# Kernel optimization log

Measured on AMD Instinct MI355X. Metric: run time of the kernel, lower is better.

The kernel has to match this reference:

```python
import jax, jax.numpy as jnp
import numpy as np

L, H, E, FFN, V, BLOCK = 8, 16, 1024, 4096, 32000, 2048
D = E // H  # head dim = 64
EPS = 1e-5
STD = 0.02

def _ln(x, g, b):
    m = jnp.mean(x, axis=-1, keepdims=True)
    v = jnp.var(x, axis=-1, keepdims=True)
    return (x - m) * jax.lax.rsqrt(v + EPS) * g + b

def setup_inputs() -> dict:
    key = jax.random.key(0)
    ks = jax.random.split(key, 12)
    n = lambda k, shape: (jax.random.normal(k, shape, dtype=jnp.float32) * STD)
    return {
        "idx": jax.random.randint(ks[0], (2, 2048), 0, V),
        "tok_emb": n(ks[1], (V, E)),
        "pos_emb": n(ks[2], (BLOCK, E)),
        # attention weights stored [in, out] so we use x @ W
        "wq": n(ks[3], (L, E, E)),
        "wk": n(ks[4], (L, E, E)),
        "wv": n(ks[5], (L, E, E)),
        "wo": n(ks[6], (L, E, E)),
        "bo": jnp.zeros((L, E), jnp.float32),
        "w1": n(ks[7], (L, E, FFN)),
        "b1": jnp.zeros((L, FFN), jnp.float32),
        "w2": n(ks[8], (L, FFN, E)),
        "b2": jnp.zeros((L, E), jnp.float32),
        "ln1_g": jnp.ones((L, E), jnp.float32),
        "ln1_b": jnp.zeros((L, E), jnp.float32),
        "ln2_g": jnp.ones((L, E), jnp.float32),
        "ln2_b": jnp.zeros((L, E), jnp.float32),
        "lnf_g": jnp.ones((E,), jnp.float32),
        "lnf_b": jnp.zeros((E,), jnp.float32),
    }

def reference(idx, tok_emb, pos_emb, wq, wk, wv, wo, bo, w1, b1, w2, b2,
              ln1_g, ln1_b, ln2_g, ln2_b, lnf_g, lnf_b):
    B, T = idx.shape
    x = tok_emb[idx] + pos_emb[:T]  # [B,T,E]
    causal = jnp.tril(jnp.ones((T, T), dtype=bool))
    scale = 1.0 / np.sqrt(D)

    def step(x, p):
        (wq_, wk_, wv_, wo_, bo_, w1_, b1_, w2_, b2_,
         g1, be1, g2, be2) = p
        h = _ln(x, g1, be1)
        q = (h @ wq_).reshape(B, T, H, D)
        k = (h @ wk_).reshape(B, T, H, D)
        v = (h @ wv_).reshape(B, T, H, D)
        scores = jnp.einsum('bthd,bshd->bhts', q, k) * scale  # [B,H,T,T]
        scores = jnp.where(causal, scores, -jnp.inf)
        w = jax.nn.softmax(scores, axis=-1)
        attn = jnp.einsum('bhts,bshd->bthd', w, v).reshape(B, T, E)
        x = x + attn @ wo_ + bo_
        h2 = _ln(x, g2, be2)
        x = x + jax.nn.relu(h2 @ w1_ + b1_) @ w2_ + b2_
        return x, None

    x, _ = jax.lax.scan(step, x, (wq, wk, wv, wo, bo, w1, b1, w2, b2,
                                  ln1_g, ln1_b, ln2_g, ln2_b))
    x = _ln(x, lnf_g, lnf_b)
    logits = x @ tok_emb.T  # tied weights
    return logits
```

## Files before the change

### kernel.cpp

```cpp
#include <hip/hip_runtime.h>
#include <hip/hip_bf16.h>
#include <cstdint>
#include <cstddef>

#define LAYERS   8
#define HEADS    16
#define EMB      1024
#define FFND     4096
#define VOCAB    32000
#define SEQ      2048
#define NBATCH   2
#define MROWS    (NBATCH*SEQ)
#define HDIM     64
#define QKVSTR   3072
#define LN_EPS   1e-5f
#define QSCALE   0.18033688011112042f

typedef __hip_bfloat16 bf16;
typedef short short8 __attribute__((ext_vector_type(8)));
typedef float f32x4  __attribute__((ext_vector_type(4)));

__device__ __forceinline__ void async_copy16(const bf16* g, bf16* l) {
  __builtin_amdgcn_global_load_lds(
      (const __attribute__((address_space(1))) void*)g,
      (__attribute__((address_space(3))) void*)l, 16, 0, 0);
}

__device__ __forceinline__ uint32_t bfbits(float x) {
  __hip_bfloat16 h = __float2bfloat16(x);
  return (uint32_t)reinterpret_cast<uint16_t&>(h);
}

struct __align__(8) B4 { bf16 a, b, c, d; };

__global__ void k_f32_to_bf16(const float* __restrict__ in, bf16* __restrict__ out, long n4) {
  long i = (long)blockIdx.x * blockDim.x + threadIdx.x;
  const long stride = (long)gridDim.x * blockDim.x;
  for (; i < n4; i += stride) {
    float4 v = reinterpret_cast<const float4*>(in)[i];
    B4 o;
    o.a = __float2bfloat16(v.x);
    o.b = __float2bfloat16(v.y);
    o.c = __float2bfloat16(v.z);
    o.d = __float2bfloat16(v.w);
    reinterpret_cast<B4*>(out)[i] = o;
  }
}

__global__ void k_embed(const int* __restrict__ idx, const float* __restrict__ tok,
                        const float* __restrict__ pos, float* __restrict__ x) {
  const int row  = blockIdx.x;
  const int tpos = row & (SEQ - 1);
  const int token = idx[row];
  const float4* te = (const float4*)(tok + (long)token * EMB);
  const float4* pe = (const float4*)(pos + (long)tpos * EMB);
  float4* xo = (float4*)(x + (long)row * EMB);
  for (int i = threadIdx.x; i < EMB / 4; i += blockDim.x) {
    float4 a = te[i], b = pe[i];
    a.x += b.x; a.y += b.y; a.z += b.z; a.w += b.w;
    xo[i] = a;
  }
}

__global__ void k_transpose_all(const float* __restrict__ wq, const float* __restrict__ wk,
                                const float* __restrict__ wv, const float* __restrict__ wo,
                                const float* __restrict__ w1, const float* __restrict__ w2,
                                bf16* __restrict__ qkvT, bf16* __restrict__ woT,
                                bf16* __restrict__ w1T, bf16* __restrict__ w2T) {
  __shared__ float tile[32][33];
  const int bid = blockIdx.x;
  const float* in; bf16* out; int K, N, bx, by;
  if (bid < 4096) {
    const int rest = bid & 1023;
    switch (bid >> 10) {
      case 0:  in = wq; out = qkvT;                 break;
      case 1:  in = wk; out = qkvT + EMB * EMB;     break;
      case 2:  in = wv; out = qkvT + 2 * EMB * EMB; break;
      default: in = wo; out = woT;                  break;
    }
    K = EMB; N = EMB; bx = rest & 31; by = rest >> 5;
  } else if (bid < 8192) {
    const int rest = bid - 4096;
    in = w1; out = w1T; K = EMB; N = FFND;
    bx = rest & 127; by = rest >> 7;
  } else {
    const int rest = bid - 8192;
    in = w2; out = w2T; K = FFND; N = EMB;
    bx = rest & 31; by = rest >> 5;
  }
  const int n0 = bx * 32, k0 = by * 32;
  const int tx = threadIdx.x, ty = threadIdx.y;
  for (int i = 0; i < 32; i += 8)
    tile[ty + i][tx] = in[(long)(k0 + ty + i) * N + n0 + tx];
  __syncthreads();
  for (int i = 0; i < 32; i += 8)
    out[(long)(n0 + ty + i) * K + k0 + tx] = __float2bfloat16(tile[tx][ty + i]);
}

__global__ void k_transpose_v(const bf16* __restrict__ v, int vstr, bf16* __restrict__ vt) {
  __shared__ bf16 tile[32][33];
  const int bh = blockIdx.z;
  const int b = bh >> 4, h = bh & 15;
  const int t0 = blockIdx.x * 32, d0 = blockIdx.y * 32;
  const int tx = threadIdx.x, ty = threadIdx.y;
  for (int i = 0; i < 32; i += 8)
    tile[ty + i][tx] = v[(long)(b * SEQ + t0 + ty + i) * vstr + h * HDIM + d0 + tx];
  __syncthreads();
  for (int i = 0; i < 32; i += 8)
    vt[(long)(bh * HDIM + d0 + ty + i) * SEQ + t0 + tx] = tile[tx][ty + i];
}

__global__ __launch_bounds__(256)
void k_layernorm(const float* __restrict__ x, const float* __restrict__ g,
                 const float* __restrict__ b, bf16* __restrict__ out) {
  const int wid  = threadIdx.x >> 6;
  const int lane = threadIdx.x & 63;
  const long row = (long)blockIdx.x * 4 + wid;
  const float4* xr = (const float4*)(x + row * EMB);
  float4 xv[4];
  float s = 0.f, sq = 0.f;
#pragma unroll
  for (int i = 0; i < 4; i++) {
    xv[i] = xr[lane + i * 64];
    s  += xv[i].x + xv[i].y + xv[i].z + xv[i].w;
    sq += xv[i].x * xv[i].x + xv[i].y * xv[i].y + xv[i].z * xv[i].z + xv[i].w * xv[i].w;
  }
#pragma unroll
  for (int m = 1; m < 64; m <<= 1) { s += __shfl_xor(s, m); sq += __shfl_xor(sq, m); }
  const float mean = s * (1.f / EMB);
  const float var  = sq * (1.f / EMB) - mean * mean;
  const float rstd = rsqrtf(var + LN_EPS);
  const float4* gv = (const float4*)g;
  const float4* bv = (const float4*)b;
  bf16* orow = out + row * EMB;
#pragma unroll
  for (int i = 0; i < 4; i++) {
    const int c4 = lane + i * 64;
    const float4 gg = gv[c4], bb = bv[c4];
    uint2 o;
    o.x = (bfbits((xv[i].y - mean) * rstd * gg.y + bb.y) << 16) |
           bfbits((xv[i].x - mean) * rstd * gg.x + bb.x);
    o.y = (bfbits((xv[i].w - mean) * rstd * gg.w + bb.w) << 16) |
           bfbits((xv[i].z - mean) * rstd * gg.z + bb.z);
    *reinterpret_cast<uint2*>(&orow[c4 * 4]) = o;
  }
}

template<int MODE>
__global__ __launch_bounds__(512, 2)
void gemm256(const bf16* __restrict__ A, const bf16* __restrict__ Bt,
             int M, int N, int K,
             bf16* __restrict__ outB, float* __restrict__ outF,
             const float* __restrict__ bias) {
  extern __shared__ __align__(16) char smem[];
  char* const smA = smem;
  char* const smB = smem + 65536;

  const int t    = threadIdx.x;
  const int lane = t & 63;
  const int wid  = t >> 6;
  const int wr   = wid >> 2;
  const int wc   = wid & 3;
  const int lrow = lane & 15;
  const int ks16 = (lane >> 4) * 16;
  const int rswz = (lrow & 7) << 4;

  int lin = blockIdx.x * gridDim.y + blockIdx.y;
  { const int nwg = gridDim.x * gridDim.y; const int per = nwg >> 3;
    lin = (lin & 7) * per + (lin >> 3); }
  const int gx8  = gridDim.x * 8;
  const int half = lin / gx8;
  const int rem  = lin - half * gx8;
  const long bm  = (long)(half * 8 + (rem & 7)) * 256;
  const long bn  = (long)(rem >> 3) * 256;
  const int NT = K >> 6;

  const int row0 = wid * 8 + (lane >> 3);
  const int col0 = ((lane & 7) ^ (lane >> 3)) * 8;
  const int row1 = row0 + 64;
  const int dst0 = wid * 1024;
  const int dst1 = 8192 + wid * 1024;
  const bf16* const gA = A  + bm * K;
  const bf16* const gB = Bt + bn * K;

  auto STG = [&](char* ring, const bf16* g_, int tile, int h) {
    char* slot = ring + (((tile << 1) + h) & 3) * 16384;
    const bf16* sb = g_ + ((long)h * 128) * K + (long)tile * 64;
    async_copy16(sb + (long)row0 * K + col0, (bf16*)(slot + dst0));
    async_copy16(sb + (long)row1 * K + col0, (bf16*)(slot + dst1));
  };
  auto LDA8 = [&](int u, int m, int kk) -> short8 {
    const int off = (m * 16 + lrow) * 128 + ((kk * 64 + ks16) ^ rswz);
    return *reinterpret_cast<const short8*>(smA + (((u << 1) + wr) & 3) * 16384 + off);
  };
  auto LDB8 = [&](int u, int n, int kk) -> short8 {
    const int off = ((wc & 1) * 64 + n * 16 + lrow) * 128 + ((kk * 64 + ks16) ^ rswz);
    return *reinterpret_cast<const short8*>(smB + (((u << 1) + (wc >> 1)) & 3) * 16384 + off);
  };
#define MF(a_, b_, c_) __builtin_amdgcn_mfma_f32_16x16x32_bf16(a_, b_, c_, 0, 0, 0)

  f32x4 acc[8][4] = {};

  STG(smB, gB, 0, 0); STG(smB, gB, 0, 1);
  STG(smA, gA, 0, 0); STG(smA, gA, 0, 1);
  STG(smB, gB, 1, 0); STG(smB, gB, 1, 1);
  asm volatile("s_waitcnt vmcnt(4)" ::: "memory");
  __builtin_amdgcn_s_barrier();

  short8 bq[4][2];
  for (int u = 0; u < NT; u++) {
#pragma unroll
    for (int n = 0; n < 4; n++) { bq[n][0] = LDB8(u, n, 0); bq[n][1] = LDB8(u, n, 1); }
    short8 a0 = LDA8(u, 0, 0), a1 = LDA8(u, 0, 1), a2 = LDA8(u, 1, 0), a3 = LDA8(u, 1, 1);
    if (u + 1 < NT) STG(smA, gA, u + 1, 0);
    __builtin_amdgcn_s_barrier();
    asm volatile("s_waitcnt lgkmcnt(0)" ::: "memory");
    __builtin_amdgcn_sched_barrier(0);
    __builtin_amdgcn_s_setprio(1);
#pragma unroll
    for (int n = 0; n < 4; n++) {
      acc[0][n] = MF(a0, bq[n][0], acc[0][n]); acc[0][n] = MF(a1, bq[n][1], acc[0][n]);
      acc[1][n] = MF(a2, bq[n][0], acc[1][n]); acc[1][n] = MF(a3, bq[n][1], acc[1][n]);
    }
    __builtin_amdgcn_s_setprio(0);
    __builtin_amdgcn_s_barrier();

    a0 = LDA8(u, 2, 0); a1 = LDA8(u, 2, 1); a2 = LDA8(u, 3, 0); a3 = LDA8(u, 3, 1);
    if (u + 1 < NT) STG(smA, gA, u + 1, 1);
    __builtin_amdgcn_s_barrier();
    asm volatile("s_waitcnt lgkmcnt(0)" ::: "memory");
    __builtin_amdgcn_sched_barrier(0);
    __builtin_amdgcn_s_setprio(1);
#pragma unroll
    for (int n = 0; n < 4; n++) {
      acc[2][n] = MF(a0, bq[n][0], acc[2][n]); acc[2][n] = MF(a1, bq[n][1], acc[2][n]);
      acc[3][n] = MF(a2, bq[n][0], acc[3][n]); acc[3][n] = MF(a3, bq[n][1], acc[3][n]);
    }
    __builtin_amdgcn_s_setprio(0);
    __builtin_amdgcn_s_barrier();

    a0 = LDA8(u, 4, 0); a1 = LDA8(u, 4, 1); a2 = LDA8(u, 5, 0); a3 = LDA8(u, 5, 1);
    if (u + 2 < NT) STG(smB, gB, u + 2, 0);
    __builtin_amdgcn_s_barrier();
    asm volatile("s_waitcnt lgkmcnt(0)" ::: "memory");
    __builtin_amdgcn_sched_barrier(0);
    __builtin_amdgcn_s_setprio(1);
#pragma unroll
    for (int n = 0; n < 4; n++) {
      acc[4][n] = MF(a0, bq[n][0], acc[4][n]); acc[4][n] = MF(a1, bq[n][1], acc[4][n]);
      acc[5][n] = MF(a2, bq[n][0], acc[5][n]); acc[5][n] = MF(a3, bq[n][1], acc[5][n]);
    }
    __builtin_amdgcn_s_setprio(0);
    __builtin_amdgcn_s_barrier();

    a0 = LDA8(u, 6, 0); a1 = LDA8(u, 6, 1); a2 = LDA8(u, 7, 0); a3 = LDA8(u, 7, 1);
    if (u + 2 < NT) STG(smB, gB, u + 2, 1);
    __builtin_amdgcn_s_barrier();
    asm volatile("s_waitcnt lgkmcnt(0)" ::: "memory");
    __builtin_amdgcn_sched_barrier(0);
    __builtin_amdgcn_s_setprio(1);
#pragma unroll
    for (int n = 0; n < 4; n++) {
      acc[6][n] = MF(a0, bq[n][0], acc[6][n]); acc[6][n] = MF(a1, bq[n][1], acc[6][n]);
      acc[7][n] = MF(a2, bq[n][0], acc[7][n]); acc[7][n] = MF(a3, bq[n][1], acc[7][n]);
    }
    __builtin_amdgcn_s_setprio(0);
    if (u + 2 < NT) { asm volatile("s_waitcnt vmcnt(4)" ::: "memory"); }
    else            { asm volatile("s_waitcnt vmcnt(0)" ::: "memory"); }
    __builtin_amdgcn_s_barrier();
  }

  const long rb = bm + wr * 128 + (lane >> 4) * 4;
  const long cb = bn + wc * 64 + lrow;
#pragma unroll
  for (int m = 0; m < 8; m++) {
#pragma unroll
    for (int n = 0; n < 4; n++) {
      const long col = cb + n * 16;
#pragma unroll
      for (int r = 0; r < 4; r++) {
        const long row = rb + m * 16 + r;
        float v = acc[m][n][r];
        if (MODE == 0) {
          if (col < EMB) v *= QSCALE;
          outB[row * N + col] = __float2bfloat16(v);
        } else if (MODE == 2) {
          v += bias[col];
          outB[row * N + col] = __float2bfloat16(v > 0.f ? v : 0.f);
        } else {
          outF[row * N + col] = v;
        }
      }
    }
  }
#undef MF
}

#define BM 128
#define BN 128
#define BK 32

__global__ __launch_bounds__(256)
void gemm_bt(const bf16* __restrict__ A, const bf16* __restrict__ Bt,
             int M, int N, int K,
             float* __restrict__ outF, const float* __restrict__ bias) {
  __shared__ __align__(16) bf16 lA[2][BM * BK];
  __shared__ __align__(16) bf16 lB[2][BN * BK];
  const int t    = threadIdx.x;
  const int lane = t & 63;
  const int wid  = t >> 6;
  const int wr   = wid >> 1;
  const int wc   = wid & 1;
  const long bm  = (long)blockIdx.y * BM;
  const long bn  = (long)blockIdx.x * BN;
  const int  kz  = blockIdx.z;
  const int  Kh  = K >> 1;

  f32x4 acc[4][4] = {};

  const long arow = t >> 2;
  const int  acol = (((t & 3) ^ ((t >> 2) & 3)) * 8);
  const bf16* gA = A  + (bm + arow) * K + kz * Kh + acol;
  const bf16* gB = Bt + (bn + arow) * K + kz * Kh + acol;
  const long astep = 64L * K;

  auto STGBT = [&](int buf, int k0) {
    async_copy16(gA + k0,         &lA[buf][wid * 512]);
    async_copy16(gA + k0 + astep, &lA[buf][wid * 512 + 2048]);
    async_copy16(gB + k0,         &lB[buf][wid * 512]);
    async_copy16(gB + k0 + astep, &lB[buf][wid * 512 + 2048]);
  };

  STGBT(0, 0);
  __syncthreads();

  int cur = 0;
  for (int k0 = 0; k0 < Kh; k0 += BK) {
    if (k0 + BK < Kh) STGBT(cur ^ 1, k0 + BK);

    const int ksel = (((lane >> 4) ^ (lane & 3)) * 8);
    short8 af[4], bfv[4];
#pragma unroll
    for (int i = 0; i < 4; i++) {
      af[i]  = *reinterpret_cast<const short8*>(&lA[cur][(wr * 64 + i * 16 + (lane & 15)) * BK + ksel]);
      bfv[i] = *reinterpret_cast<const short8*>(&lB[cur][(wc * 64 + i * 16 + (lane & 15)) * BK + ksel]);
    }
#pragma unroll
    for (int i = 0; i < 4; i++)
#pragma unroll
      for (int j = 0; j < 4; j++)
        acc[i][j] = __builtin_amdgcn_mfma_f32_16x16x32_bf16(af[i], bfv[j], acc[i][j], 0, 0, 0);
    __syncthreads();
    cur ^= 1;
  }

  const long rbase = bm + wr * 64 + (lane >> 4) * 4;
  const long cbase = bn + wc * 64 + (lane & 15);
#pragma unroll
  for (int i = 0; i < 4; i++) {
#pragma unroll
    for (int j = 0; j < 4; j++) {
      const long col = cbase + j * 16;
      const float bv = kz ? 0.f : bias[col];
#pragma unroll
      for (int r = 0; r < 4; r++) {
        const long row = rbase + i * 16 + r;
        unsafeAtomicAdd(&outF[row * N + col], acc[i][j][r] + bv);
      }
    }
  }
}

__global__ __launch_bounds__(256)
void k_attn(const bf16* __restrict__ qkv, const bf16* __restrict__ vt, bf16* __restrict__ o) {
  const int bh = blockIdx.y;
  const int qt = (bh & 16) ? blockIdx.x : (gridDim.x - 1 - blockIdx.x);
  const int b  = bh >> 4;
  const int h  = bh & 15;
  const int t0b = qt * 128;
  const int tid = threadIdx.x;
  const int w    = tid >> 6;
  const int lane = tid & 63;
  const int lg = lane >> 4;
  const int li = lane & 15;
  const int t0w = t0b + w * 32;

  __shared__ __align__(16) bf16 Kl[2][64 * 64];
  __shared__ __align__(16) bf16 Vl[2][64 * 64];
  __shared__ __align__(16) bf16 Pl[4][32 * 64];

  const bf16* qbase = qkv + (long)(b * SEQ) * QKVSTR + h * HDIM;
  const bf16* kbase = qkv + (long)(b * SEQ) * QKVSTR + EMB + h * HDIM;
  const bf16* vbase = vt + (long)bh * HDIM * SEQ;

  short8 qf[2][2];
#pragma unroll
  for (int f = 0; f < 2; f++) {
    const bf16* qrow = qbase + (long)(t0w + f * 16 + li) * QKVSTR;
    qf[f][0] = *reinterpret_cast<const short8*>(&qrow[lg * 8]);
    qf[f][1] = *reinterpret_cast<const short8*>(&qrow[32 + lg * 8]);
  }

  f32x4 oacc[2][4] = {};
  float mrow[2] = {-1e30f, -1e30f}, lrow[2] = {0.f, 0.f};

  const int nkt = (t0b >> 6) + 1;
  const int l8  = lane >> 3;
  const int sl8 = ((lane & 7) ^ l8) * 8;

  char* const Pw = (char*)&Pl[w][0];
  const int pswz = (li & 7) << 4;

#pragma unroll
  for (int sh = 0; sh < 2; sh++) {
    const int r = sh * 32 + w * 8 + l8;
    async_copy16(kbase + (long)r * QKVSTR + sl8, &Kl[0][(sh * 32 + w * 8) * 64]);
    async_copy16(vbase + (long)r * SEQ + sl8,    &Vl[0][(sh * 32 + w * 8) * 64]);
  }
  __syncthreads();

  int cur = 0;
  for (int kt = 0; kt <= nkt; kt++) {
    const int s0 = kt * 64;
    if (kt < nkt) {
      const int s0n = s0 + 64;
      bf16* Kn = &Kl[cur ^ 1][0];
      bf16* Vn = &Vl[cur ^ 1][0];
#pragma unroll
      for (int sh = 0; sh < 2; sh++) {
        const int r = sh * 32 + w * 8 + l8;
        async_copy16(kbase + (long)(s0n + r) * QKVSTR + sl8, Kn + (sh * 32 + w * 8) * 64);
        async_copy16(vbase + (long)r * SEQ + s0n + sl8,      Vn + (sh * 32 + w * 8) * 64);
      }
    }

    f32x4 s[2][4] = {};
#pragma unroll
    for (int kk = 0; kk < 2; kk++)
#pragma unroll
      for (int sf = 0; sf < 4; sf++) {
        const short8 kf = *reinterpret_cast<const short8*>(
            &Kl[cur][(sf * 16 + li) * 64 + ((((kk << 2) | lg) ^ (li & 7)) * 8)]);
        s[0][sf] = __builtin_amdgcn_mfma_f32_16x16x32_bf16(kf, qf[0][kk], s[0][sf], 0, 0, 0);
        s[1][sf] = __builtin_amdgcn_mfma_f32_16x16x32_bf16(kf, qf[1][kk], s[1][sf], 0, 0, 0);
      }

    const bool diag = (kt >= nkt - 1);
    if (diag) {
#pragma unroll
      for (int f = 0; f < 2; f++)
#pragma unroll
        for (int sf = 0; sf < 4; sf++)
#pragma unroll
          for (int r = 0; r < 4; r++)
            if (s0 + sf * 16 + lg * 4 + r > t0w + f * 16 + li) s[f][sf][r] = -1e30f;
    }

#pragma unroll
    for (int f = 0; f < 2; f++) {
      float mx = -1e30f;
#pragma unroll
      for (int sf = 0; sf < 4; sf++)
        mx = fmaxf(mx, fmaxf(fmaxf(s[f][sf][0], s[f][sf][1]), fmaxf(s[f][sf][2], s[f][sf][3])));
      mx = fmaxf(mx, __shfl_xor(mx, 16));
      mx = fmaxf(mx, __shfl_xor(mx, 32));
      if (__any(mx > mrow[f] + 8.f)) {
        const float mnew = fmaxf(mrow[f], mx);
        const float alpha = exp2f(mrow[f] - mnew);
        mrow[f] = mnew;
        lrow[f] *= alpha;
#pragma unroll
        for (int d = 0; d < 4; d++)
#pragma unroll
          for (int r = 0; r < 4; r++) oacc[f][d][r] *= alpha;
      }
      float rs = 0.f;
#pragma unroll
      for (int sf = 0; sf < 4; sf++)
#pragma unroll
        for (int r = 0; r < 4; r++) {
          const float pv = exp2f(s[f][sf][r] - mrow[f]);
          s[f][sf][r] = pv;
          rs += pv;
        }
      rs += __shfl_xor(rs, 16);
      rs += __shfl_xor(rs, 32);
      lrow[f] += rs;

#pragma unroll
      for (int sf = 0; sf < 4; sf++) {
        uint2 pw2;
        pw2.x = (bfbits(s[f][sf][1]) << 16) | bfbits(s[f][sf][0]);
        pw2.y = (bfbits(s[f][sf][3]) << 16) | bfbits(s[f][sf][2]);
        *reinterpret_cast<uint2*>(Pw + (f * 16 + li) * 128 + ((sf * 32 + lg * 8) ^ pswz)) = pw2;
      }
    }

#pragma unroll
    for (int kk = 0; kk < 2; kk++) {
      const short8 pb0 = *reinterpret_cast<const short8*>(
          Pw + li * 128 + ((kk * 64 + lg * 16) ^ pswz));
      const short8 pb1 = *reinterpret_cast<const short8*>(
          Pw + (16 + li) * 128 + ((kk * 64 + lg * 16) ^ pswz));
#pragma unroll
      for (int d = 0; d < 4; d++) {
        const short8 vf = *reinterpret_cast<const short8*>(
            &Vl[cur][(d * 16 + li) * 64 + ((((kk << 2) | lg) ^ (li & 7)) * 8)]);
        oacc[0][d] = __builtin_amdgcn_mfma_f32_16x16x32_bf16(vf, pb0, oacc[0][d], 0, 0, 0);
        oacc[1][d] = __builtin_amdgcn_mfma_f32_16x16x32_bf16(vf, pb1, oacc[1][d], 0, 0, 0);
      }
    }

    __syncthreads();
    cur ^= 1;
  }

#pragma unroll
  for (int f = 0; f < 2; f++) {
    const float inv = 1.f / lrow[f];
    bf16* orow = o + (long)(b * SEQ + t0w + f * 16 + li) * EMB + h * HDIM;
#pragma unroll
    for (int d = 0; d < 4; d++) {
      uint2 ow;
      ow.x = (bfbits(oacc[f][d][1] * inv) << 16) | bfbits(oacc[f][d][0] * inv);
      ow.y = (bfbits(oacc[f][d][3] * inv) << 16) | bfbits(oacc[f][d][2] * inv);
      *reinterpret_cast<uint2*>(&orow[d * 16 + lg * 4]) = ow;
    }
  }
}

extern "C" void kernel_launch(void* const* d_in, const int* in_sizes, int n_in,
                              void* d_out, int out_size, void* d_ws, size_t ws_size,
                              hipStream_t stream) {
  (void)in_sizes; (void)n_in; (void)out_size; (void)ws_size;
  const int*   idx = (const int*)  d_in[0];
  const float* tok = (const float*)d_in[1];
  const float* pos = (const float*)d_in[2];
  const float* wq  = (const float*)d_in[3];
  const float* wk  = (const float*)d_in[4];
  const float* wv  = (const float*)d_in[5];
  const float* wo  = (const float*)d_in[6];
  const float* bo  = (const float*)d_in[7];
  const float* w1  = (const float*)d_in[8];
  const float* b1  = (const float*)d_in[9];
  const float* w2  = (const float*)d_in[10];
  const float* b2  = (const float*)d_in[11];
  const float* g1  = (const float*)d_in[12];
  const float* be1 = (const float*)d_in[13];
  const float* g2  = (const float*)d_in[14];
  const float* be2 = (const float*)d_in[15];
  const float* gf  = (const float*)d_in[16];
  const float* bef = (const float*)d_in[17];
  float* out = (float*)d_out;

  (void)hipFuncSetAttribute((const void*)gemm256<0>, hipFuncAttributeMaxDynamicSharedMemorySize, 131072);
  (void)hipFuncSetAttribute((const void*)gemm256<2>, hipFuncAttributeMaxDynamicSharedMemorySize, 131072);
  (void)hipFuncSetAttribute((const void*)gemm256<3>, hipFuncAttributeMaxDynamicSharedMemorySize, 131072);

  char* p = (char*)d_ws;
  auto take = [&p](size_t bytes) { char* r = p; p += (bytes + 255) & ~(size_t)255; return r; };
  float* xf   = (float*)take((size_t)MROWS * EMB * 4);
  bf16*  hb   = (bf16*) take((size_t)MROWS * EMB * 2);
  bf16*  qkvb = (bf16*) take((size_t)MROWS * QKVSTR * 2);
  bf16*  vtb  = (bf16*) take((size_t)MROWS * EMB * 2);
  bf16*  ab   = (bf16*) take((size_t)MROWS * EMB * 2);
  bf16*  fb   = (bf16*) take((size_t)MROWS * FFND * 2);
  bf16*  wqkvT= (bf16*) take((size_t)QKVSTR * EMB * 2);
  bf16*  woT  = (bf16*) take((size_t)EMB * EMB * 2);
  bf16*  w1T  = (bf16*) take((size_t)FFND * EMB * 2);
  bf16*  w2T  = (bf16*) take((size_t)EMB * FFND * 2);
  bf16*  tokT = (bf16*) take((size_t)VOCAB * EMB * 2);

  k_f32_to_bf16<<<2048, 256, 0, stream>>>(tok, tokT, (long)VOCAB * EMB / 4);
  k_embed<<<MROWS, 256, 0, stream>>>(idx, tok, pos, xf);

  const dim3 tb(32, 8);

  for (int l = 0; l < LAYERS; l++) {
    const size_t we = (size_t)l * EMB * EMB;
    const size_t wfo = (size_t)l * EMB * FFND;
    k_transpose_all<<<12288, tb, 0, stream>>>(
        wq + we, wk + we, wv + we, wo + we, w1 + wfo, w2 + wfo, wqkvT, woT, w1T, w2T);

    k_layernorm<<<MROWS / 4, 256, 0, stream>>>(xf, g1 + l * EMB, be1 + l * EMB, hb);
    gemm256<0><<<dim3(QKVSTR / 256, MROWS / 256), 512, 131072, stream>>>(
        hb, wqkvT, MROWS, QKVSTR, EMB, qkvb, nullptr, nullptr);
    k_transpose_v<<<dim3(SEQ / 32, HDIM / 32, NBATCH * HEADS), tb, 0, stream>>>(qkvb + 2 * EMB, QKVSTR, vtb);
    k_attn<<<dim3(SEQ / 128, NBATCH * HEADS), 256, 0, stream>>>(qkvb, vtb, ab);
    gemm_bt<<<dim3(EMB / BN, MROWS / BM, 2), 256, 0, stream>>>(ab, woT, MROWS, EMB, EMB, xf, bo + l * EMB);
    k_layernorm<<<MROWS / 4, 256, 0, stream>>>(xf, g2 + l * EMB, be2 + l * EMB, hb);
    gemm256<2><<<dim3(FFND / 256, MROWS / 256), 512, 131072, stream>>>(
        hb, w1T, MROWS, FFND, EMB, fb, nullptr, b1 + l * FFND);
    gemm_bt<<<dim3(EMB / BN, MROWS / BM, 2), 256, 0, stream>>>(fb, w2T, MROWS, EMB, FFND, xf, b2 + l * EMB);
  }

  k_layernorm<<<MROWS / 4, 256, 0, stream>>>(xf, gf, bef, hb);
  gemm256<3><<<dim3(VOCAB / 256, MROWS / 256), 512, 131072, stream>>>(
      hb, tokT, MROWS, VOCAB, EMB, nullptr, out, nullptr);
}
```

Baseline: 2.557 ms.

## Halve GEMM barrier phases and process two N tiles per block in vocab GEMM

The 256x256 GEMM main loop now does two compute phases per K tile instead of four. Each phase loads eight A fragments, issues both A or both B half-tile prefetches together, and runs 32 MFMAs, which halves the number of barriers per iteration. A new NSUB template parameter lets one block loop over several consecutive 256-wide N tiles. The vocabulary projection uses it with two tiles per block, cutting the grid from 125 to 63 column groups. The price is more live A-fragment registers under a tight launch-bound budget, which risks spills, and a serial second tile in the logits GEMM that may change wave-quantization behaviour.

```diff
diff --git a/kernel.cpp b/kernel.cpp
--- a/kernel.cpp
+++ b/kernel.cpp
@@ -146,7 +146,7 @@
   }
 }
 
-template<int MODE>
+template<int MODE, int NSUB>
 __global__ __launch_bounds__(512, 2)
 void gemm256(const bf16* __restrict__ A, const bf16* __restrict__ Bt,
              int M, int N, int K,
@@ -172,7 +172,7 @@
   const int half = lin / gx8;
   const int rem  = lin - half * gx8;
   const long bm  = (long)(half * 8 + (rem & 7)) * 256;
-  const long bn  = (long)(rem >> 3) * 256;
+  const long bn0 = (long)(rem >> 3) * (256 * NSUB);
   const int NT = K >> 6;
 
   const int row0 = wid * 8 + (lane >> 3);
@@ -180,8 +180,7 @@
   const int row1 = row0 + 64;
   const int dst0 = wid * 1024;
   const int dst1 = 8192 + wid * 1024;
-  const bf16* const gA = A  + bm * K;
-  const bf16* const gB = Bt + bn * K;
+  const bf16* const gA = A + bm * K;
 
   auto STG = [&](char* ring, const bf16* g_, int tile, int h) {
     char* slot = ring + (((tile << 1) + h) & 3) * 16384;
@@ -199,96 +198,80 @@
   };
 #define MF(a_, b_, c_) __builtin_amdgcn_mfma_f32_16x16x32_bf16(a_, b_, c_, 0, 0, 0)
 
-  f32x4 acc[8][4] = {};
-
-  STG(smB, gB, 0, 0); STG(smB, gB, 0, 1);
-  STG(smA, gA, 0, 0); STG(smA, gA, 0, 1);
-  STG(smB, gB, 1, 0); STG(smB, gB, 1, 1);
-  asm volatile("s_waitcnt vmcnt(4)" ::: "memory");
-  __builtin_amdgcn_s_barrier();
-
-  short8 bq[4][2];
-  for (int u = 0; u < NT; u++) {
-#pragma unroll
-    for (int n = 0; n < 4; n++) { bq[n][0] = LDB8(u, n, 0); bq[n][1] = LDB8(u, n, 1); }
-    short8 a0 = LDA8(u, 0, 0), a1 = LDA8(u, 0, 1), a2 = LDA8(u, 1, 0), a3 = LDA8(u, 1, 1);
-    if (u + 1 < NT) STG(smA, gA, u + 1, 0);
+  for (int v = 0; v < NSUB; v++) {
+    const long bn = bn0 + (long)v * 256;
+    if (NSUB > 1 && bn >= N) break;
+    const bf16* const gB = Bt + bn * K;
+
+    f32x4 acc[8][4] = {};
+
+    STG(smB, gB, 0, 0); STG(smB, gB, 0, 1);
+    STG(smA, gA, 0, 0); STG(smA, gA, 0, 1);
+    STG(smB, gB, 1, 0); STG(smB, gB, 1, 1);
+    asm volatile("s_waitcnt vmcnt(4)" ::: "memory");
     __builtin_amdgcn_s_barrier();
-    asm volatile("s_waitcnt lgkmcnt(0)" ::: "memory");
-    __builtin_amdgcn_sched_barrier(0);
-    __builtin_amdgcn_s_setprio(1);
-#pragma unroll
-    for (int n = 0; n < 4; n++) {
-      acc[0][n] = MF(a0, bq[n][0], acc[0][n]); acc[0][n] = MF(a1, bq[n][1], acc[0][n]);
-      acc[1][n] = MF(a2, bq[n][0], acc[1][n]); acc[1][n] = MF(a3, bq[n][1], acc[1][n]);
-    }
-    __builtin_amdgcn_s_setprio(0);
-    __builtin_amdgcn_s_barrier();
-
-    a0 = LDA8(u, 2, 0); a1 = LDA8(u, 2, 1); a2 = LDA8(u, 3, 0); a3 = LDA8(u, 3, 1);
-    if (u + 1 < NT) STG(smA, gA, u + 1, 1);
-    __builtin_amdgcn_s_barrier();
-    asm volatile("s_waitcnt lgkmcnt(0)" ::: "memory");
-    __builtin_amdgcn_sched_barrier(0);
-    __builtin_amdgcn_s_setprio(1);
-#pragma unroll
-    for (int n = 0; n < 4; n++) {
-      acc[2][n] = MF(a0, bq[n][0], acc[2][n]); acc[2][n] = MF(a1, bq[n][1], acc[2][n]);
-      acc[3][n] = MF(a2, bq[n][0], acc[3][n]); acc[3][n] = MF(a3, bq[n][1], acc[3][n]);
-    }
-    __builtin_amdgcn_s_setprio(0);
-    __builtin_amdgcn_s_barrier();
-
-    a0 = LDA8(u, 4, 0); a1 = LDA8(u, 4, 1); a2 = LDA8(u, 5, 0); a3 = LDA8(u, 5, 1);
-    if (u + 2 < NT) STG(smB, gB, u + 2, 0);
-    __builtin_amdgcn_s_barrier();
-    asm volatile("s_waitcnt lgkmcnt(0)" ::: "memory");
-    __builtin_amdgcn_sched_barrier(0);
-    __builtin_amdgcn_s_setprio(1);
-#pragma unroll
-    for (int n = 0; n < 4; n++) {
-      acc[4][n] = MF(a0, bq[n][0], acc[4][n]); acc[4][n] = MF(a1, bq[n][1], acc[4][n]);
-      acc[5][n] = MF(a2, bq[n][0], acc[5][n]); acc[5][n] = MF(a3, bq[n][1], acc[5][n]);
-    }
-    __builtin_amdgcn_s_setprio(0);
-    __builtin_amdgcn_s_barrier();
-
-    a0 = LDA8(u, 6, 0); a1 = LDA8(u, 6, 1); a2 = LDA8(u, 7, 0); a3 = LDA8(u, 7, 1);
-    if (u + 2 < NT) STG(smB, gB, u + 2, 1);
-    __builtin_amdgcn_s_barrier();
-    asm volatile("s_waitcnt lgkmcnt(0)" ::: "memory");
-    __builtin_amdgcn_sched_barrier(0);
-    __builtin_amdgcn_s_setprio(1);
-#pragma unroll
-    for (int n = 0; n < 4; n++) {
-      acc[6][n] = MF(a0, bq[n][0], acc[6][n]); acc[6][n] = MF(a1, bq[n][1], acc[6][n]);
-      acc[7][n] = MF(a2, bq[n][0], acc[7][n]); acc[7][n] = MF(a3, bq[n][1], acc[7][n]);
-    }
-    __builtin_amdgcn_s_setprio(0);
-    if (u + 2 < NT) { asm volatile("s_waitcnt vmcnt(4)" ::: "memory"); }
-    else            { asm volatile("s_waitcnt vmcnt(0)" ::: "memory"); }
-    __builtin_amdgcn_s_barrier();
-  }
-
-  const long rb = bm + wr * 128 + (lane >> 4) * 4;
-  const long cb = bn + wc * 64 + lrow;
-#pragma unroll
-  for (int m = 0; m < 8; m++) {
-#pragma unroll
-    for (int n = 0; n < 4; n++) {
-      const long col = cb + n * 16;
-#pragma unroll
-      for (int r = 0; r < 4; r++) {
-        const long row = rb + m * 16 + r;
-        float v = acc[m][n][r];
-        if (MODE == 0) {
-          if (col < EMB) v *= QSCALE;
-          outB[row * N + col] = __float2bfloat16(v);
-        } else if (MODE == 2) {
-          v += bias[col];
-          outB[row * N + col] = __float2bfloat16(v > 0.f ? v : 0.f);
-        } else {
-          outF[row * N + col] = v;
+
+    short8 bq[4][2];
+    for (int u = 0; u < NT; u++) {
+#pragma unroll
+      for (int n = 0; n < 4; n++) { bq[n][0] = LDB8(u, n, 0); bq[n][1] = LDB8(u, n, 1); }
+      short8 a0 = LDA8(u, 0, 0), a1 = LDA8(u, 0, 1), a2 = LDA8(u, 1, 0), a3 = LDA8(u, 1, 1);
+      short8 a4 = LDA8(u, 2, 0), a5 = LDA8(u, 2, 1), a6 = LDA8(u, 3, 0), a7 = LDA8(u, 3, 1);
+      if (u + 1 < NT) { STG(smA, gA, u + 1, 0); STG(smA, gA, u + 1, 1); }
+      __builtin_amdgcn_s_barrier();
+      asm volatile("s_waitcnt lgkmcnt(0)" ::: "memory");
+      __builtin_amdgcn_sched_barrier(0);
+      __builtin_amdgcn_s_setprio(1);
+#pragma unroll
+      for (int n = 0; n < 4; n++) {
+        acc[0][n] = MF(a0, bq[n][0], acc[0][n]); acc[0][n] = MF(a1, bq[n][1], acc[0][n]);
+        acc[1][n] = MF(a2, bq[n][0], acc[1][n]); acc[1][n] = MF(a3, bq[n][1], acc[1][n]);
+        acc[2][n] = MF(a4, bq[n][0], acc[2][n]); acc[2][n] = MF(a5, bq[n][1], acc[2][n]);
+        acc[3][n] = MF(a6, bq[n][0], acc[3][n]); acc[3][n] = MF(a7, bq[n][1], acc[3][n]);
+      }
+      __builtin_amdgcn_s_setprio(0);
+      __builtin_amdgcn_s_barrier();
+
+      a0 = LDA8(u, 4, 0); a1 = LDA8(u, 4, 1); a2 = LDA8(u, 5, 0); a3 = LDA8(u, 5, 1);
+      a4 = LDA8(u, 6, 0); a5 = LDA8(u, 6, 1); a6 = LDA8(u, 7, 0); a7 = LDA8(u, 7, 1);
+      if (u + 2 < NT) { STG(smB, gB, u + 2, 0); STG(smB, gB, u + 2, 1); }
+      __builtin_amdgcn_s_barrier();
+      asm volatile("s_waitcnt lgkmcnt(0)" ::: "memory");
+      __builtin_amdgcn_sched_barrier(0);
+      __builtin_amdgcn_s_setprio(1);
+#pragma unroll
+      for (int n = 0; n < 4; n++) {
+        acc[4][n] = MF(a0, bq[n][0], acc[4][n]); acc[4][n] = MF(a1, bq[n][1], acc[4][n]);
+        acc[5][n] = MF(a2, bq[n][0], acc[5][n]); acc[5][n] = MF(a3, bq[n][1], acc[5][n]);
+        acc[6][n] = MF(a4, bq[n][0], acc[6][n]); acc[6][n] = MF(a5, bq[n][1], acc[6][n]);
+        acc[7][n] = MF(a6, bq[n][0], acc[7][n]); acc[7][n] = MF(a7, bq[n][1], acc[7][n]);
+      }
+      __builtin_amdgcn_s_setprio(0);
+      if (u + 2 < NT) { asm volatile("s_waitcnt vmcnt(4)" ::: "memory"); }
+      else            { asm volatile("s_waitcnt vmcnt(0)" ::: "memory"); }
+      __builtin_amdgcn_s_barrier();
+    }
+
+    const long rb = bm + wr * 128 + (lane >> 4) * 4;
+    const long cb = bn + wc * 64 + lrow;
+#pragma unroll
+    for (int m = 0; m < 8; m++) {
+#pragma unroll
+      for (int n = 0; n < 4; n++) {
+        const long col = cb + n * 16;
+#pragma unroll
+        for (int r = 0; r < 4; r++) {
+          const long row = rb + m * 16 + r;
+          float vv = acc[m][n][r];
+          if (MODE == 0) {
+            if (col < EMB) vv *= QSCALE;
+            outB[row * N + col] = __float2bfloat16(vv);
+          } else if (MODE == 2) {
+            vv += bias[col];
+            outB[row * N + col] = __float2bfloat16(vv > 0.f ? vv : 0.f);
+          } else {
+            outF[row * N + col] = vv;
+          }
         }
       }
     }
@@ -553,9 +536,9 @@
   const float* bef = (const float*)d_in[17];
   float* out = (float*)d_out;
 
-  (void)hipFuncSetAttribute((const void*)gemm256<0>, hipFuncAttributeMaxDynamicSharedMemorySize, 131072);
-  (void)hipFuncSetAttribute((const void*)gemm256<2>, hipFuncAttributeMaxDynamicSharedMemorySize, 131072);
-  (void)hipFuncSetAttribute((const void*)gemm256<3>, hipFuncAttributeMaxDynamicSharedMemorySize, 131072);
+  (void)hipFuncSetAttribute((const void*)gemm256<0,1>, hipFuncAttributeMaxDynamicSharedMemorySize, 131072);
+  (void)hipFuncSetAttribute((const void*)gemm256<2,1>, hipFuncAttributeMaxDynamicSharedMemorySize, 131072);
+  (void)hipFuncSetAttribute((const void*)gemm256<3,2>, hipFuncAttributeMaxDynamicSharedMemorySize, 131072);
 
   char* p = (char*)d_ws;
   auto take = [&p](size_t bytes) { char* r = p; p += (bytes + 255) & ~(size_t)255; return r; };
@@ -583,18 +566,18 @@
         wq + we, wk + we, wv + we, wo + we, w1 + wfo, w2 + wfo, wqkvT, woT, w1T, w2T);
 
     k_layernorm<<<MROWS / 4, 256, 0, stream>>>(xf, g1 + l * EMB, be1 + l * EMB, hb);
-    gemm256<0><<<dim3(QKVSTR / 256, MROWS / 256), 512, 131072, stream>>>(
+    gemm256<0,1><<<dim3(QKVSTR / 256, MROWS / 256), 512, 131072, stream>>>(
         hb, wqkvT, MROWS, QKVSTR, EMB, qkvb, nullptr, nullptr);
     k_transpose_v<<<dim3(SEQ / 32, HDIM / 32, NBATCH * HEADS), tb, 0, stream>>>(qkvb + 2 * EMB, QKVSTR, vtb);
     k_attn<<<dim3(SEQ / 128, NBATCH * HEADS), 256, 0, stream>>>(qkvb, vtb, ab);
     gemm_bt<<<dim3(EMB / BN, MROWS / BM, 2), 256, 0, stream>>>(ab, woT, MROWS, EMB, EMB, xf, bo + l * EMB);
     k_layernorm<<<MROWS / 4, 256, 0, stream>>>(xf, g2 + l * EMB, be2 + l * EMB, hb);
-    gemm256<2><<<dim3(FFND / 256, MROWS / 256), 512, 131072, stream>>>(
+    gemm256<2,1><<<dim3(FFND / 256, MROWS / 256), 512, 131072, stream>>>(
         hb, w1T, MROWS, FFND, EMB, fb, nullptr, b1 + l * FFND);
     gemm_bt<<<dim3(EMB / BN, MROWS / BM, 2), 256, 0, stream>>>(fb, w2T, MROWS, EMB, FFND, xf, b2 + l * EMB);
   }
 
   k_layernorm<<<MROWS / 4, 256, 0, stream>>>(xf, gf, bef, hb);
-  gemm256<3><<<dim3(VOCAB / 256, MROWS / 256), 512, 131072, stream>>>(
+  gemm256<3,2><<<dim3(63, MROWS / 256), 512, 131072, stream>>>(
       hb, tokT, MROWS, VOCAB, EMB, nullptr, out, nullptr);
 }
```

New measurement: 2.554 ms. Within noise of the previous version (-0.1%).

## Fuse V transpose into QKV GEMM epilogue, restructure main loop, add persistent logits GEMM

Applied to the files above, without the earlier changes.

The QKV GEMM epilogue now writes the V columns directly in transposed per-head layout, so the separate V-transpose kernel and its extra global round trip are gone. The gemm256 main loop is regrouped into two larger phases per K-tile with fewer barriers, which holds more A fragments in registers. A new logits GEMM has each workgroup compute two adjacent 256-column tiles in turn, streaming B continuously, to cut the partial last wave on the 125-column-tile vocab grid. The trade-offs are higher register pressure, scattered 8-byte V stores, and more complex tile-index logic.

```diff
diff --git a/kernel.cpp b/kernel.cpp
--- a/kernel.cpp
+++ b/kernel.cpp
@@ -97,19 +97,6 @@
     out[(long)(n0 + ty + i) * K + k0 + tx] = __float2bfloat16(tile[tx][ty + i]);
 }
 
-__global__ void k_transpose_v(const bf16* __restrict__ v, int vstr, bf16* __restrict__ vt) {
-  __shared__ bf16 tile[32][33];
-  const int bh = blockIdx.z;
-  const int b = bh >> 4, h = bh & 15;
-  const int t0 = blockIdx.x * 32, d0 = blockIdx.y * 32;
-  const int tx = threadIdx.x, ty = threadIdx.y;
-  for (int i = 0; i < 32; i += 8)
-    tile[ty + i][tx] = v[(long)(b * SEQ + t0 + ty + i) * vstr + h * HDIM + d0 + tx];
-  __syncthreads();
-  for (int i = 0; i < 32; i += 8)
-    vt[(long)(bh * HDIM + d0 + ty + i) * SEQ + t0 + tx] = tile[tx][ty + i];
-}
-
 __global__ __launch_bounds__(256)
 void k_layernorm(const float* __restrict__ x, const float* __restrict__ g,
                  const float* __restrict__ b, bf16* __restrict__ out) {
@@ -150,8 +137,8 @@
 __global__ __launch_bounds__(512, 2)
 void gemm256(const bf16* __restrict__ A, const bf16* __restrict__ Bt,
              int M, int N, int K,
-             bf16* __restrict__ outB, float* __restrict__ outF,
-             const float* __restrict__ bias) {
+             bf16* __restrict__ outB, const float* __restrict__ bias,
+             bf16* __restrict__ vt_out) {
   extern __shared__ __align__(16) char smem[];
   char* const smA = smem;
   char* const smB = smem + 65536;
@@ -180,7 +167,7 @@
   const int row1 = row0 + 64;
   const int dst0 = wid * 1024;
   const int dst1 = 8192 + wid * 1024;
-  const bf16* const gA = A  + bm * K;
+  const bf16* const gA = A + bm * K;
   const bf16* const gB = Bt + bn * K;
 
   auto STG = [&](char* ring, const bf16* g_, int tile, int h) {
@@ -212,7 +199,8 @@
 #pragma unroll
     for (int n = 0; n < 4; n++) { bq[n][0] = LDB8(u, n, 0); bq[n][1] = LDB8(u, n, 1); }
     short8 a0 = LDA8(u, 0, 0), a1 = LDA8(u, 0, 1), a2 = LDA8(u, 1, 0), a3 = LDA8(u, 1, 1);
-    if (u + 1 < NT) STG(smA, gA, u + 1, 0);
+    short8 a4 = LDA8(u, 2, 0), a5 = LDA8(u, 2, 1), a6 = LDA8(u, 3, 0), a7 = LDA8(u, 3, 1);
+    if (u + 1 < NT) { STG(smA, gA, u + 1, 0); STG(smA, gA, u + 1, 1); }
     __builtin_amdgcn_s_barrier();
     asm volatile("s_waitcnt lgkmcnt(0)" ::: "memory");
     __builtin_amdgcn_sched_barrier(0);
@@ -221,78 +209,195 @@
     for (int n = 0; n < 4; n++) {
       acc[0][n] = MF(a0, bq[n][0], acc[0][n]); acc[0][n] = MF(a1, bq[n][1], acc[0][n]);
       acc[1][n] = MF(a2, bq[n][0], acc[1][n]); acc[1][n] = MF(a3, bq[n][1], acc[1][n]);
+      acc[2][n] = MF(a4, bq[n][0], acc[2][n]); acc[2][n] = MF(a5, bq[n][1], acc[2][n]);
+      acc[3][n] = MF(a6, bq[n][0], acc[3][n]); acc[3][n] = MF(a7, bq[n][1], acc[3][n]);
     }
     __builtin_amdgcn_s_setprio(0);
     __builtin_amdgcn_s_barrier();
 
-    a0 = LDA8(u, 2, 0); a1 = LDA8(u, 2, 1); a2 = LDA8(u, 3, 0); a3 = LDA8(u, 3, 1);
-    if (u + 1 < NT) STG(smA, gA, u + 1, 1);
+    a0 = LDA8(u, 4, 0); a1 = LDA8(u, 4, 1); a2 = LDA8(u, 5, 0); a3 = LDA8(u, 5, 1);
+    a4 = LDA8(u, 6, 0); a5 = LDA8(u, 6, 1); a6 = LDA8(u, 7, 0); a7 = LDA8(u, 7, 1);
+    if (u + 2 < NT) { STG(smB, gB, u + 2, 0); STG(smB, gB, u + 2, 1); }
     __builtin_amdgcn_s_barrier();
     asm volatile("s_waitcnt lgkmcnt(0)" ::: "memory");
     __builtin_amdgcn_sched_barrier(0);
     __builtin_amdgcn_s_setprio(1);
 #pragma unroll
     for (int n = 0; n < 4; n++) {
-      acc[2][n] = MF(a0, bq[n][0], acc[2][n]); acc[2][n] = MF(a1, bq[n][1], acc[2][n]);
-      acc[3][n] = MF(a2, bq[n][0], acc[3][n]); acc[3][n] = MF(a3, bq[n][1], acc[3][n]);
+      acc[4][n] = MF(a0, bq[n][0], acc[4][n]); acc[4][n] = MF(a1, bq[n][1], acc[4][n]);
+      acc[5][n] = MF(a2, bq[n][0], acc[5][n]); acc[5][n] = MF(a3, bq[n][1], acc[5][n]);
+      acc[6][n] = MF(a4, bq[n][0], acc[6][n]); acc[6][n] = MF(a5, bq[n][1], acc[6][n]);
+      acc[7][n] = MF(a6, bq[n][0], acc[7][n]); acc[7][n] = MF(a7, bq[n][1], acc[7][n]);
     }
     __builtin_amdgcn_s_setprio(0);
+    if (u + 2 < NT) { asm volatile("s_waitcnt vmcnt(4)" ::: "memory"); }
+    else            { asm volatile("s_waitcnt vmcnt(0)" ::: "memory"); }
     __builtin_amdgcn_s_barrier();
-
-    a0 = LDA8(u, 4, 0); a1 = LDA8(u, 4, 1); a2 = LDA8(u, 5, 0); a3 = LDA8(u, 5, 1);
-    if (u + 2 < NT) STG(smB, gB, u + 2, 0);
+  }
+
+  const long rb = bm + wr * 128 + (lane >> 4) * 4;
+  const long cb = bn + wc * 64 + lrow;
+#pragma unroll
+  for (int m = 0; m < 8; m++) {
+#pragma unroll
+    for (int n = 0; n < 4; n++) {
+      const long col = cb + n * 16;
+      if (MODE == 0 && col >= 2 * EMB) {
+        const int  dc = (int)(col - 2 * EMB);
+        const long t0 = rb + m * 16;
+        const long vr = ((t0 >> 11) * HEADS + (dc >> 6)) * (long)HDIM + (dc & 63);
+        uint2 pv;
+        pv.x = (bfbits(acc[m][n][1]) << 16) | bfbits(acc[m][n][0]);
+        pv.y = (bfbits(acc[m][n][3]) << 16) | bfbits(acc[m][n][2]);
+        *reinterpret_cast<uint2*>(&vt_out[vr * SEQ + (t0 & (SEQ - 1))]) = pv;
+      } else {
+#pragma unroll
+        for (int r = 0; r < 4; r++) {
+          const long row = rb + m * 16 + r;
+          float vv = acc[m][n][r];
+          if (MODE == 0) {
+            if (col < EMB) vv *= QSCALE;
+            outB[row * N + col] = __float2bfloat16(vv);
+          } else {
+            vv += bias[col];
+            outB[row * N + col] = __float2bfloat16(vv > 0.f ? vv : 0.f);
+          }
+        }
+      }
+    }
+  }
+#undef MF
+}
+
+__global__ __launch_bounds__(512, 2)
+void gemm_logits(const bf16* __restrict__ A, const bf16* __restrict__ Bt,
+                 int M, int N, int K, float* __restrict__ outF) {
+  extern __shared__ __align__(16) char smem[];
+  char* const smA = smem;
+  char* const smB = smem + 65536;
+
+  const int t    = threadIdx.x;
+  const int lane = t & 63;
+  const int wid  = t >> 6;
+  const int wr   = wid >> 2;
+  const int wc   = wid & 3;
+  const int lrow = lane & 15;
+  const int ks16 = (lane >> 4) * 16;
+  const int rswz = (lrow & 7) << 4;
+
+  int lin = blockIdx.x * gridDim.y + blockIdx.y;
+  { const int nwg = gridDim.x * gridDim.y; const int per = nwg >> 3;
+    lin = (lin & 7) * per + (lin >> 3); }
+  const int gx8  = gridDim.x * 8;
+  const int half = lin / gx8;
+  const int rem  = lin - half * gx8;
+  const long bm  = (long)(half * 8 + (rem & 7)) * 256;
+  const long bn0 = (long)(rem >> 3) * 512;
+  const long bn1 = bn0 + 256;
+  const int NT = K >> 6;
+  const int TT = (bn1 < N) ? (NT * 2) : NT;
+
+  const int row0 = wid * 8 + (lane >> 3);
+  const int col0 = ((lane & 7) ^ (lane >> 3)) * 8;
+  const int row1 = row0 + 64;
+  const int dst0 = wid * 1024;
+  const int dst1 = 8192 + wid * 1024;
+  const bf16* const gA  = A + bm * K;
+  const bf16* const gB0 = Bt + bn0 * K;
+  const bf16* const gB1 = Bt + bn1 * K;
+
+  auto STG2 = [&](char* ring, const bf16* src, int slotTile, int h) {
+    char* slot = ring + (((slotTile << 1) + h) & 3) * 16384;
+    const bf16* sb = src + ((long)h * 128) * K + (long)(slotTile & (NT - 1)) * 64;
+    async_copy16(sb + (long)row0 * K + col0, (bf16*)(slot + dst0));
+    async_copy16(sb + (long)row1 * K + col0, (bf16*)(slot + dst1));
+  };
+  auto LDA8 = [&](int u, int m, int kk) -> short8 {
+    const int off = (m * 16 + lrow) * 128 + ((kk * 64 + ks16) ^ rswz);
+    return *reinterpret_cast<const short8*>(smA + (((u << 1) + wr) & 3) * 16384 + off);
+  };
+  auto LDB8 = [&](int u, int n, int kk) -> short8 {
+    const int off = ((wc & 1) * 64 + n * 16 + lrow) * 128 + ((kk * 64 + ks16) ^ rswz);
+    return *reinterpret_cast<const short8*>(smB + (((u << 1) + (wc >> 1)) & 3) * 16384 + off);
+  };
+#define MF(a_, b_, c_) __builtin_amdgcn_mfma_f32_16x16x32_bf16(a_, b_, c_, 0, 0, 0)
+
+  f32x4 acc[8][4] = {};
+  const long rb = bm + wr * 128 + (lane >> 4) * 4;
+
+  auto epi = [&](long bn) {
+    const long cb = bn + wc * 64 + lrow;
+#pragma unroll
+    for (int m = 0; m < 8; m++)
+#pragma unroll
+      for (int n = 0; n < 4; n++) {
+        const long col = cb + n * 16;
+#pragma unroll
+        for (int r = 0; r < 4; r++)
+          outF[(rb + m * 16 + r) * N + col] = acc[m][n][r];
+      }
+  };
+
+  STG2(smB, gB0, 0, 0); STG2(smB, gB0, 0, 1);
+  STG2(smA, gA,  0, 0); STG2(smA, gA,  0, 1);
+  STG2(smB, gB0, 1, 0); STG2(smB, gB0, 1, 1);
+  asm volatile("s_waitcnt vmcnt(4)" ::: "memory");
+  __builtin_amdgcn_s_barrier();
+
+  short8 bq[4][2];
+  for (int u = 0; u < TT; u++) {
+#pragma unroll
+    for (int n = 0; n < 4; n++) { bq[n][0] = LDB8(u, n, 0); bq[n][1] = LDB8(u, n, 1); }
+    short8 a0 = LDA8(u, 0, 0), a1 = LDA8(u, 0, 1), a2 = LDA8(u, 1, 0), a3 = LDA8(u, 1, 1);
+    short8 a4 = LDA8(u, 2, 0), a5 = LDA8(u, 2, 1), a6 = LDA8(u, 3, 0), a7 = LDA8(u, 3, 1);
+    if (u + 1 < TT) { STG2(smA, gA, u + 1, 0); STG2(smA, gA, u + 1, 1); }
     __builtin_amdgcn_s_barrier();
     asm volatile("s_waitcnt lgkmcnt(0)" ::: "memory");
     __builtin_amdgcn_sched_barrier(0);
     __builtin_amdgcn_s_setprio(1);
 #pragma unroll
     for (int n = 0; n < 4; n++) {
-      acc[4][n] = MF(a0, bq[n][0], acc[4][n]); acc[4][n] = MF(a1, bq[n][1], acc[4][n]);
-      acc[5][n] = MF(a2, bq[n][0], acc[5][n]); acc[5][n] = MF(a3, bq[n][1], acc[5][n]);
+      acc[0][n] = MF(a0, bq[n][0], acc[0][n]); acc[0][n] = MF(a1, bq[n][1], acc[0][n]);
+      acc[1][n] = MF(a2, bq[n][0], acc[1][n]); acc[1][n] = MF(a3, bq[n][1], acc[1][n]);
+      acc[2][n] = MF(a4, bq[n][0], acc[2][n]); acc[2][n] = MF(a5, bq[n][1], acc[2][n]);
+      acc[3][n] = MF(a6, bq[n][0], acc[3][n]); acc[3][n] = MF(a7, bq[n][1], acc[3][n]);
     }
     __builtin_amdgcn_s_setprio(0);
     __builtin_amdgcn_s_barrier();
 
-    a0 = LDA8(u, 6, 0); a1 = LDA8(u, 6, 1); a2 = LDA8(u, 7, 0); a3 = LDA8(u, 7, 1);
-    if (u + 2 < NT) STG(smB, gB, u + 2, 1);
+    a0 = LDA8(u, 4, 0); a1 = LDA8(u, 4, 1); a2 = LDA8(u, 5, 0); a3 = LDA8(u, 5, 1);
+    a4 = LDA8(u, 6, 0); a5 = LDA8(u, 6, 1); a6 = LDA8(u, 7, 0); a7 = LDA8(u, 7, 1);
+    if (u + 2 < TT) {
+      const bf16* bs = ((u + 2) >= NT) ? gB1 : gB0;
+      STG2(smB, bs, u + 2, 0); STG2(smB, bs, u + 2, 1);
+    }
     __builtin_amdgcn_s_barrier();
     asm volatile("s_waitcnt lgkmcnt(0)" ::: "memory");
     __builtin_amdgcn_sched_barrier(0);
     __builtin_amdgcn_s_setprio(1);
 #pragma unroll
     for (int n = 0; n < 4; n++) {
-      acc[6][n] = MF(a0, bq[n][0], acc[6][n]); acc[6][n] = MF(a1, bq[n][1], acc[6][n]);
-      acc[7][n] = MF(a2, bq[n][0], acc[7][n]); acc[7][n] = MF(a3, bq[n][1], acc[7][n]);
+      acc[4][n] = MF(a0, bq[n][0], acc[4][n]); acc[4][n] = MF(a1, bq[n][1], acc[4][n]);
+      acc[5][n] = MF(a2, bq[n][0], acc[5][n]); acc[5][n] = MF(a3, bq[n][1], acc[5][n]);
+      acc[6][n] = MF(a4, bq[n][0], acc[6][n]); acc[6][n] = MF(a5, bq[n][1], acc[6][n]);
+      acc[7][n] = MF(a6, bq[n][0], acc[7][n]); acc[7][n] = MF(a7, bq[n][1], acc[7][n]);
     }
     __builtin_amdgcn_s_setprio(0);
-    if (u + 2 < NT) { asm volatile("s_waitcnt vmcnt(4)" ::: "memory"); }
+    if (u + 2 < TT) { asm volatile("s_waitcnt vmcnt(4)" ::: "memory"); }
     else            { asm volatile("s_waitcnt vmcnt(0)" ::: "memory"); }
     __builtin_amdgcn_s_barrier();
-  }
-
-  const long rb = bm + wr * 128 + (lane >> 4) * 4;
-  const long cb = bn + wc * 64 + lrow;
-#pragma unroll
-  for (int m = 0; m < 8; m++) {
-#pragma unroll
-    for (int n = 0; n < 4; n++) {
-      const long col = cb + n * 16;
-#pragma unroll
-      for (int r = 0; r < 4; r++) {
-        const long row = rb + m * 16 + r;
-        float v = acc[m][n][r];
-        if (MODE == 0) {
-          if (col < EMB) v *= QSCALE;
-          outB[row * N + col] = __float2bfloat16(v);
-        } else if (MODE == 2) {
-          v += bias[col];
-          outB[row * N + col] = __float2bfloat16(v > 0.f ? v : 0.f);
-        } else {
-          outF[row * N + col] = v;
-        }
-      }
-    }
-  }
+
+    if (u == NT - 1 && TT > NT) {
+      epi(bn0);
+#pragma unroll
+      for (int m = 0; m < 8; m++)
+#pragma unroll
+        for (int n = 0; n < 4; n++)
+#pragma unroll
+          for (int r = 0; r < 4; r++) acc[m][n][r] = 0.f;
+    }
+  }
+  epi(TT > NT ? bn1 : bn0);
 #undef MF
 }
 
@@ -555,7 +660,7 @@
 
   (void)hipFuncSetAttribute((const void*)gemm256<0>, hipFuncAttributeMaxDynamicSharedMemorySize, 131072);
   (void)hipFuncSetAttribute((const void*)gemm256<2>, hipFuncAttributeMaxDynamicSharedMemorySize, 131072);
-  (void)hipFuncSetAttribute((const void*)gemm256<3>, hipFuncAttributeMaxDynamicSharedMemorySize, 131072);
+  (void)hipFuncSetAttribute((const void*)gemm_logits, hipFuncAttributeMaxDynamicSharedMemorySize, 131072);
 
   char* p = (char*)d_ws;
   auto take = [&p](size_t bytes) { char* r = p; p += (bytes + 255) & ~(size_t)255; return r; };
@@ -584,17 +689,16 @@
 
     k_layernorm<<<MROWS / 4, 256, 0, stream>>>(xf, g1 + l * EMB, be1 + l * EMB, hb);
     gemm256<0><<<dim3(QKVSTR / 256, MROWS / 256), 512, 131072, stream>>>(
-        hb, wqkvT, MROWS, QKVSTR, EMB, qkvb, nullptr, nullptr);
-    k_transpose_v<<<dim3(SEQ / 32, HDIM / 32, NBATCH * HEADS), tb, 0, stream>>>(qkvb + 2 * EMB, QKVSTR, vtb);
+        hb, wqkvT, MROWS, QKVSTR, EMB, qkvb, nullptr, vtb);
     k_attn<<<dim3(SEQ / 128, NBATCH * HEADS), 256, 0, stream>>>(qkvb, vtb, ab);
     gemm_bt<<<dim3(EMB / BN, MROWS / BM, 2), 256, 0, stream>>>(ab, woT, MROWS, EMB, EMB, xf, bo + l * EMB);
     k_layernorm<<<MROWS / 4, 256, 0, stream>>>(xf, g2 + l * EMB, be2 + l * EMB, hb);
     gemm256<2><<<dim3(FFND / 256, MROWS / 256), 512, 131072, stream>>>(
-        hb, w1T, MROWS, FFND, EMB, fb, nullptr, b1 + l * FFND);
+        hb, w1T, MROWS, FFND, EMB, fb, b1 + l * FFND, nullptr);
     gemm_bt<<<dim3(EMB / BN, MROWS / BM, 2), 256, 0, stream>>>(fb, w2T, MROWS, EMB, FFND, xf, b2 + l * EMB);
   }
 
   k_layernorm<<<MROWS / 4, 256, 0, stream>>>(xf, gf, bef, hb);
-  gemm256<3><<<dim3(VOCAB / 256, MROWS / 256), 512, 131072, stream>>>(
-      hb, tokT, MROWS, VOCAB, EMB, nullptr, out, nullptr);
-}
+  gemm_logits<<<dim3(63, MROWS / 256), 512, 131072, stream>>>(
+      hb, tokT, MROWS, VOCAB, EMB, out);
+}
```

After: 2.665 ms. +4.2%, slower.
